# Optimization experiments

Measured on AMD Instinct MI355X. Metric: run time of the kernel, lower is better.

Reference implementation:

```python
import jax, jax.numpy as jnp
import numpy as np


def _deg2_idx(cpg):
    # pairs (c1, c2) with c1 <= c2, c2 inner loop -> matches torch nested loop order
    i, j = np.triu_indices(cpg)
    return i, j


def _deg3_idx(cpg):
    # triples (c1, c2, c3) with c1 <= c2 <= c3, same nesting order as torch loops
    t = np.array([(a, b, c) for a in range(cpg) for b in range(a, cpg) for c in range(b, cpg)], dtype=np.int32)
    return t[:, 0], t[:, 1], t[:, 2]


def setup_inputs() -> dict:
    key = jax.random.key(0)
    ks = jax.random.split(key, 7)
    B, C, H, W = 16, 256, 56, 56
    G = 32
    cpg = C // G  # 8
    n2 = cpg * (cpg + 1) // 2  # 36
    n3 = sum((i + 1) * (i + 2) // 2 for i in range(cpg))  # 120
    x = jax.random.normal(ks[0], (B, C, H, W), dtype=jnp.float32)
    w1 = jax.random.normal(ks[1], (G, cpg, cpg), dtype=jnp.float32) * 0.1
    b1 = jax.random.normal(ks[2], (G, cpg), dtype=jnp.float32) * 0.1
    w2 = jax.random.normal(ks[3], (G, cpg, n2), dtype=jnp.float32) * 0.1
    b2 = jax.random.normal(ks[4], (G, cpg), dtype=jnp.float32) * 0.1
    w3 = jax.random.normal(ks[5], (G, cpg, n3), dtype=jnp.float32) * 0.1
    b3 = jax.random.normal(ks[6], (G, cpg), dtype=jnp.float32) * 0.1
    return {"x": x, "w1": w1, "b1": b1, "w2": w2, "b2": b2, "w3": w3, "b3": b3}


def reference(x, w1, b1, w2, b2, w3, b3):
    B, C, H, W = x.shape
    G, cpg, _ = w1.shape
    xg = x.reshape(B, G, cpg, H, W)  # [B, G, cpg, H, W]

    i2, j2 = _deg2_idx(cpg)
    a3, b3i, c3 = _deg3_idx(cpg)

    # polynomial feature expansion (per group, vectorized over all dims)
    d2 = xg[:, :, i2] * xg[:, :, j2]                        # [B, G, n2, H, W]
    d3 = xg[:, :, a3] * xg[:, :, b3i] * xg[:, :, c3]        # [B, G, n3, H, W]

    # grouped 1x1 convs as per-group matmuls, summed (matches output += conv(...))
    out = jnp.einsum('bgkhw,gok->bgohw', xg, w1) + b1[None, :, :, None, None]
    out = out + jnp.einsum('bgkhw,gok->bgohw', d2, w2) + b2[None, :, :, None, None]
    out = out + jnp.einsum('bgkhw,gok->bgohw', d3, w3) + b3[None, :, :, None, None]
    return out.reshape(B, C, H, W)
```

## Files before the change

### kernel.cpp

```cpp
#include <hip/hip_runtime.h>

#define CPG 8
#define NGRP 32
#define NB 16
#define HW 3136
#define HU 784
#define N2 36
#define N3 120

typedef float vfloat4 __attribute__((ext_vector_type(4)));

__host__ __device__ constexpr int idx2(int i, int j) {
    return i * CPG - i * (i - 1) / 2 + (j - i);
}
__host__ __device__ constexpr int idx3(int a, int b, int c) {
    int base = 0;
    for (int t = 0; t < a; ++t) { int m = CPG - t; base += m * (m + 1) / 2; }
    for (int t = a; t < b; ++t) base += CPG - t;
    return base + (c - b);
}

__device__ inline vfloat4 splat4(float s) { return (vfloat4){s, s, s, s}; }

#define ACCUM(F, T) do {                                                       \
    const vfloat4 wa = *reinterpret_cast<const vfloat4*>(&wt[(F)][0]);         \
    const vfloat4 wb = *reinterpret_cast<const vfloat4*>(&wt[(F)][4]);         \
    acc[0] += wa.x * (T); acc[1] += wa.y * (T);                                \
    acc[2] += wa.z * (T); acc[3] += wa.w * (T);                                \
    acc[4] += wb.x * (T); acc[5] += wb.y * (T);                                \
    acc[6] += wb.z * (T); acc[7] += wb.w * (T);                                \
} while (0)

#define FENCE() __builtin_amdgcn_sched_barrier(0)

__global__ __launch_bounds__(256, 6) void hoaf_kernel(
    const float* __restrict__ x,
    const float* __restrict__ w1, const float* __restrict__ b1,
    const float* __restrict__ w2, const float* __restrict__ b2,
    const float* __restrict__ w3, const float* __restrict__ b3,
    float* __restrict__ out)
{
    __shared__ __align__(16) float wt[165][8];

    const int tid   = threadIdx.x;
    const int g     = blockIdx.x;
    const int b     = blockIdx.y;
    const int chunk = blockIdx.z;

    for (int idx = tid; idx < 165 * 8; idx += 256) {
        const int f = idx >> 3, o = idx & 7;
        const int ch = g * CPG + o;
        float v;
        if (f < 8)        v = w1[ch * CPG + f];
        else if (f < 44)  v = w2[ch * N2 + (f - 8)];
        else if (f < 164) v = w3[ch * N3 + (f - 44)];
        else              v = b1[ch] + b2[ch] + b3[ch];
        wt[f][o] = v;
    }
    __syncthreads();

    const int q = tid + chunk * 256;
    if (q >= HU) return;

    const vfloat4 b_lo = *reinterpret_cast<const vfloat4*>(&wt[164][0]);
    const vfloat4 b_hi = *reinterpret_cast<const vfloat4*>(&wt[164][4]);

    const size_t base = ((size_t)(b * NGRP + g) * CPG) * HW;
    const vfloat4* x4 = (const vfloat4*)(x + base);
    vfloat4*       o4 = (vfloat4*)(out + base);

    vfloat4 xv[CPG];
#pragma unroll
    for (int c = 0; c < CPG; ++c) xv[c] = x4[(size_t)c * HU + q];

    vfloat4 acc[CPG];
    acc[0] = splat4(b_lo.x); acc[1] = splat4(b_lo.y);
    acc[2] = splat4(b_lo.z); acc[3] = splat4(b_lo.w);
    acc[4] = splat4(b_hi.x); acc[5] = splat4(b_hi.y);
    acc[6] = splat4(b_hi.z); acc[7] = splat4(b_hi.w);

#pragma unroll
    for (int k = 0; k < CPG; k += 2) {
        ACCUM(k, xv[k]);
        ACCUM(k + 1, xv[k + 1]);
        FENCE();
    }

#pragma unroll
    for (int i = 0; i < CPG; ++i) {
#pragma unroll
        for (int j = i; j < CPG; ++j) {
            const vfloat4 p = xv[i] * xv[j];
            ACCUM(8 + idx2(i, j), p);
#pragma unroll
            for (int a = 0; a <= i; ++a) {
                const vfloat4 t = xv[a] * p;
                ACCUM(44 + idx3(a, i, j), t);
            }
            FENCE();
        }
    }

#pragma unroll
    for (int o = 0; o < CPG; ++o) o4[(size_t)o * HU + q] = acc[o];
}

extern "C" void kernel_launch(void* const* d_in, const int* in_sizes, int n_in,
                              void* d_out, int out_size, void* d_ws, size_t ws_size,
                              hipStream_t stream) {
    const float* x  = (const float*)d_in[0];
    const float* w1 = (const float*)d_in[1];
    const float* b1 = (const float*)d_in[2];
    const float* w2 = (const float*)d_in[3];
    const float* b2 = (const float*)d_in[4];
    const float* w3 = (const float*)d_in[5];
    const float* b3 = (const float*)d_in[6];
    float* out = (float*)d_out;

    dim3 grid(NGRP, NB, 4);
    dim3 block(256);
    hoaf_kernel<<<grid, block, 0, stream>>>(x, w1, b1, w2, b2, w3, b3, out);
}
```

Baseline: 158.6 us.

## Pre-pack weights in workspace and read them via uniform scalar loads instead of LDS

After: 147.1 us. -7.3%, faster.

```diff
diff --git a/kernel.cpp b/kernel.cpp
--- a/kernel.cpp
+++ b/kernel.cpp
@@ -7,6 +7,8 @@
 #define HU 784
 #define N2 36
 #define N3 120
+#define NF 165
+#define WSTRIDE (NF * CPG)
 
 typedef float vfloat4 __attribute__((ext_vector_type(4)));
 
@@ -21,6 +23,84 @@
 }
 
 __device__ inline vfloat4 splat4(float s) { return (vfloat4){s, s, s, s}; }
+
+__global__ __launch_bounds__(256) void prep_weights(
+    const float* __restrict__ w1, const float* __restrict__ b1,
+    const float* __restrict__ w2, const float* __restrict__ b2,
+    const float* __restrict__ w3, const float* __restrict__ b3,
+    float* __restrict__ ws)
+{
+    const int g = blockIdx.x;
+    for (int idx = threadIdx.x; idx < WSTRIDE; idx += 256) {
+        const int f = idx >> 3, o = idx & 7;
+        const int ch = g * CPG + o;
+        float v;
+        if (f < 8)        v = w1[ch * CPG + f];
+        else if (f < 44)  v = w2[ch * N2 + (f - 8)];
+        else if (f < 164) v = w3[ch * N3 + (f - 44)];
+        else              v = b1[ch] + b2[ch] + b3[ch];
+        ws[g * WSTRIDE + idx] = v;
+    }
+}
+
+#define ACCUMS(F, T) do {                                                    \
+    const float w0 = wp[(F) * 8 + 0], w1_ = wp[(F) * 8 + 1];                 \
+    const float w2_ = wp[(F) * 8 + 2], w3_ = wp[(F) * 8 + 3];                \
+    const float w4_ = wp[(F) * 8 + 4], w5_ = wp[(F) * 8 + 5];                \
+    const float w6_ = wp[(F) * 8 + 6], w7_ = wp[(F) * 8 + 7];                \
+    acc[0] += w0  * (T); acc[1] += w1_ * (T);                                \
+    acc[2] += w2_ * (T); acc[3] += w3_ * (T);                                \
+    acc[4] += w4_ * (T); acc[5] += w5_ * (T);                                \
+    acc[6] += w6_ * (T); acc[7] += w7_ * (T);                                \
+} while (0)
+
+__global__ __launch_bounds__(256, 2) void hoaf_sload(
+    const float* __restrict__ x,
+    const float* __restrict__ ws,
+    float* __restrict__ out)
+{
+    const int tid   = threadIdx.x;
+    const int g     = blockIdx.x;
+    const int b     = blockIdx.y;
+    const int chunk = blockIdx.z;
+
+    const int q = tid + chunk * 256;
+    if (q >= HU) return;
+
+    const float* __restrict__ wp = ws + g * WSTRIDE;
+
+    const size_t base = ((size_t)(b * NGRP + g) * CPG) * HW;
+    const vfloat4* x4 = (const vfloat4*)(x + base);
+    vfloat4*       o4 = (vfloat4*)(out + base);
+
+    vfloat4 xv[CPG];
+#pragma unroll
+    for (int c = 0; c < CPG; ++c) xv[c] = x4[(size_t)c * HU + q];
+
+    vfloat4 acc[CPG];
+#pragma unroll
+    for (int o = 0; o < CPG; ++o) acc[o] = splat4(wp[164 * 8 + o]);
+
+#pragma unroll
+    for (int k = 0; k < CPG; ++k) ACCUMS(k, xv[k]);
+
+#pragma unroll
+    for (int i = 0; i < CPG; ++i) {
+#pragma unroll
+        for (int j = i; j < CPG; ++j) {
+            const vfloat4 p = xv[i] * xv[j];
+            ACCUMS(8 + idx2(i, j), p);
+#pragma unroll
+            for (int a = 0; a <= i; ++a) {
+                const vfloat4 t = xv[a] * p;
+                ACCUMS(44 + idx3(a, i, j), t);
+            }
+        }
+    }
+
+#pragma unroll
+    for (int o = 0; o < CPG; ++o) o4[(size_t)o * HU + q] = acc[o];
+}
 
 #define ACCUM(F, T) do {                                                       \
     const vfloat4 wa = *reinterpret_cast<const vfloat4*>(&wt[(F)][0]);         \
@@ -30,10 +110,9 @@
     acc[4] += wb.x * (T); acc[5] += wb.y * (T);                                \
     acc[6] += wb.z * (T); acc[7] += wb.w * (T);                                \
 } while (0)
-
 #define FENCE() __builtin_amdgcn_sched_barrier(0)
 
-__global__ __launch_bounds__(256, 6) void hoaf_kernel(
+__global__ __launch_bounds__(256, 4) void hoaf_lds(
     const float* __restrict__ x,
     const float* __restrict__ w1, const float* __restrict__ b1,
     const float* __restrict__ w2, const float* __restrict__ b2,
@@ -116,8 +195,16 @@
     const float* w3 = (const float*)d_in[5];
     const float* b3 = (const float*)d_in[6];
     float* out = (float*)d_out;
+    float* ws  = (float*)d_ws;
 
     dim3 grid(NGRP, NB, 4);
     dim3 block(256);
-    hoaf_kernel<<<grid, block, 0, stream>>>(x, w1, b1, w2, b2, w3, b3, out);
-}
+
+    const size_t ws_needed = (size_t)NGRP * WSTRIDE * sizeof(float);
+    if (ws != nullptr && ws_size >= ws_needed) {
+        prep_weights<<<dim3(NGRP), dim3(256), 0, stream>>>(w1, b1, w2, b2, w3, b3, ws);
+        hoaf_sload<<<grid, block, 0, stream>>>(x, ws, out);
+    } else {
+        hoaf_lds<<<grid, block, 0, stream>>>(x, w1, b1, w2, b2, w3, b3, out);
+    }
+}
```
